# Kernel optimization log

Measured on AMD Instinct MI355X. Metric: run time of the kernel, lower is better.

Reference implementation:

```python
import jax, jax.numpy as jnp
import numpy as np

C = 343.0      # speed of sound (init kwarg c)
F = 16         # number of frequency channels (len(omega))
H = 128        # MLP hidden width
N = 131072     # collocation points


def _mlp(coords, W1, b1, W2, b2, W3, b3):
    # coords: [..., 3] -> [..., 2F] (first F = real part, last F = imag part)
    h = jnp.tanh(coords @ W1 + b1)
    h = jnp.tanh(h @ W2 + b2)
    return h @ W3 + b3


def setup_inputs() -> dict:
    key = jax.random.key(0)
    ks = jax.random.split(key, 4)
    inputs = jax.random.normal(ks[0], (N, 3), dtype=jnp.float32)
    # omega = 2*pi*f for f = 100..1600 Hz (matches init kwarg list)
    omega = 2.0 * jnp.pi * 100.0 * jnp.arange(1, F + 1, dtype=jnp.float32)
    s_in = 1.0 / np.sqrt(3.0)
    s_h = 1.0 / np.sqrt(float(H))
    W1 = jax.random.normal(ks[1], (3, H), dtype=jnp.float32) * s_in
    b1 = jnp.zeros((H,), dtype=jnp.float32)
    W2 = jax.random.normal(ks[2], (H, H), dtype=jnp.float32) * s_h
    b2 = jnp.zeros((H,), dtype=jnp.float32)
    W3 = jax.random.normal(ks[3], (H, 2 * F), dtype=jnp.float32) * s_h
    b3 = jnp.zeros((2 * F,), dtype=jnp.float32)
    return {"inputs": inputs, "omega": omega, "W1": W1, "b1": b1,
            "W2": W2, "b2": b2, "W3": W3, "b3": b3}


def reference(inputs, omega, W1, b1, W2, b2, W3, b3):
    # Pointwise network R^3 -> R^{2F} (real/imag stacked).
    f = lambda c3: _mlp(c3, W1, b1, W2, b2, W3, b3)

    # u: complex pressure per point per frequency, [N, F]
    out = _mlp(inputs, W1, b1, W2, b2, W3, b3)           # [N, 2F]
    u = out[:, :F] + 1j * out[:, F:]

    # Full spatial Hessian per point via forward-over-reverse AD (fused
    # replacement for the torch per-channel autograd.grad loop).
    hess = jax.vmap(jax.jacfwd(jax.jacrev(f)))(inputs)   # [N, 2F, 3, 3]
    lap_ri = jnp.einsum('nfii->nf', hess)                # diagonal trace = Laplacian
    lap = lap_ri[:, :F] + 1j * lap_ri[:, F:]             # [N, F] complex

    # PDE residual skips channel 0, exactly as the torch loop (i+1 indexing).
    k2 = (omega[1:] / C) ** 2                            # [F-1]
    residual = lap[:, 1:] + k2 * u[:, 1:]                # [N, F-1]

    # mean over channels then over batch == global mean of |residual|^2
    return jnp.mean(jnp.abs(residual) ** 2)
```

## Files before the change

### kernel.cpp

```cpp
#include <hip/hip_runtime.h>
#include <math.h>

#ifndef __has_builtin
#define __has_builtin(x) 0
#endif

#define NPTS   131072
#define FCH    16
#define CSND   343.0f
#define PB     32
#define BLOCK  256
#define GRID   512
#define NBLK   (NPTS / PB)

typedef _Float16 half8 __attribute__((ext_vector_type(8)));
typedef _Float16 half2v __attribute__((ext_vector_type(2)));
typedef float    f32x4 __attribute__((ext_vector_type(4)));

static __device__ __forceinline__ unsigned pack2(float a, float b) {
#if __has_builtin(__builtin_amdgcn_cvt_pkrtz)
  return __builtin_bit_cast(unsigned, __builtin_amdgcn_cvt_pkrtz(a, b));
#else
  half2v v; v[0] = (_Float16)a; v[1] = (_Float16)b;
  return __builtin_bit_cast(unsigned, v);
#endif
}

static __device__ __forceinline__ float mytanh(float x) {
#if __has_builtin(__builtin_amdgcn_exp2f)
  float e = __builtin_amdgcn_exp2f(2.885390082f * x);
#else
  float e = __expf(2.0f * x);
#endif
  return fmaf(-2.0f, __builtin_amdgcn_rcpf(e + 1.0f), 1.0f);
}


__global__ __launch_bounds__(BLOCK, 2) void helmholtz_kernel(
    const float* __restrict__ x,
    const float* __restrict__ omega,
    const float* __restrict__ W1,
    const float* __restrict__ b1,
    const float* __restrict__ W2,
    const float* __restrict__ b2,
    const float* __restrict__ W3,
    const float* __restrict__ b3,
    float* __restrict__ out)
{
  __shared__ unsigned s_A[160 * 64];
  __shared__ unsigned s_HG[32 * 128];

  const int tid  = threadIdx.x;
  const int w    = tid >> 6;
  const int l    = tid & 63;
  const int col  = l & 15;
  const int quad = l >> 4;
  const int ph   = w >> 1;
  const int nh   = w & 1;

  const int pA = tid >> 4;
  const int g  = tid & 15;
  float wx[8], wy[8], wz[8], bB[8];
#pragma unroll
  for (int u = 0; u < 8; u++) {
    int unit = 8 * g + u;
    wx[u] = W1[unit]; wy[u] = W1[128 + unit]; wz[u] = W1[256 + unit];
    bB[u] = b1[unit];
  }

  half8 w2f[4][4];
#pragma unroll
  for (int t4 = 0; t4 < 4; t4++) {
    const int n = 64 * nh + 16 * t4 + col;
#pragma unroll
    for (int ks = 0; ks < 4; ks++) {
      half8 f;
#pragma unroll
      for (int j8 = 0; j8 < 8; j8++)
        f[j8] = (_Float16)W2[(ks * 32 + (quad << 3) + j8) * 128 + n];
      w2f[t4][ks] = f;
    }
  }
  half8 w3f[4];
#pragma unroll
  for (int ks = 0; ks < 4; ks++) {
    half8 f;
#pragma unroll
    for (int j8 = 0; j8 < 8; j8++) {
      int kap = ks * 32 + (quad << 3) + j8;
      int q   = kap >> 1;
      int j   = 64 * (q >> 5) + 32 * ((q >> 4) & 1) + 16 * (kap & 1) + (q & 15);
      f[j8] = (_Float16)W3[j * 32 + 16 * nh + col];
    }
    w3f[ks] = f;
  }

  float b2r[4];
#pragma unroll
  for (int t4 = 0; t4 < 4; t4++) b2r[t4] = b2[64 * nh + 16 * t4 + col];
  float k2v = 0.0f;
  if (col >= 1) {
    float om = omega[col] * (1.0f / CSND);
    k2v = om * om;
  }
  const float b3v = b3[16 * nh + col];

  float wsum = 0.0f;
  float xr[2][3];

  auto loadX = [&](int blk) {
    const float* xb = x + (size_t)blk * PB * 3;
#pragma unroll
    for (int hp = 0; hp < 2; hp++) {
      int p = pA + 16 * hp;
      xr[hp][0] = xb[3 * p]; xr[hp][1] = xb[3 * p + 1]; xr[hp][2] = xb[3 * p + 2];
    }
  };

  auto phaseA = [&]() {
    const int cbase = (g ^ pA) << 2;
    float wq[8];
#pragma unroll
    for (int u = 0; u < 8; u++)
      wq[u] = fmaf(wx[u], wx[u], fmaf(wy[u], wy[u], wz[u] * wz[u]));
#pragma unroll
    for (int hp = 0; hp < 2; hp++) {
      int p = pA + 16 * hp;
      float x0 = xr[hp][0], x1 = xr[hp][1], x2 = xr[hp][2];
      float t[8], s[8];
#pragma unroll
      for (int u = 0; u < 8; u++) {
        float z = fmaf(x0, wx[u], fmaf(x1, wy[u], fmaf(x2, wz[u], bB[u])));
        t[u] = mytanh(z);
        s[u] = 1.0f - t[u] * t[u];
      }
      uint4 q;
      q = make_uint4(pack2(t[0], t[1]), pack2(t[2], t[3]),
                     pack2(t[4], t[5]), pack2(t[6], t[7]));
      *(uint4*)&s_A[(p)       * 64 + cbase] = q;
      q = make_uint4(pack2(s[0]*wx[0], s[1]*wx[1]), pack2(s[2]*wx[2], s[3]*wx[3]),
                     pack2(s[4]*wx[4], s[5]*wx[5]), pack2(s[6]*wx[6], s[7]*wx[7]));
      *(uint4*)&s_A[(32 + p)  * 64 + cbase] = q;
      q = make_uint4(pack2(s[0]*wy[0], s[1]*wy[1]), pack2(s[2]*wy[2], s[3]*wy[3]),
                     pack2(s[4]*wy[4], s[5]*wy[5]), pack2(s[6]*wy[6], s[7]*wy[7]));
      *(uint4*)&s_A[(64 + p)  * 64 + cbase] = q;
      q = make_uint4(pack2(s[0]*wz[0], s[1]*wz[1]), pack2(s[2]*wz[2], s[3]*wz[3]),
                     pack2(s[4]*wz[4], s[5]*wz[5]), pack2(s[6]*wz[6], s[7]*wz[7]));
      *(uint4*)&s_A[(96 + p)  * 64 + cbase] = q;
      float c[8];
#pragma unroll
      for (int u = 0; u < 8; u++) c[u] = -2.0f * t[u] * s[u] * wq[u];
      q = make_uint4(pack2(c[0], c[1]), pack2(c[2], c[3]),
                     pack2(c[4], c[5]), pack2(c[6], c[7]));
      *(uint4*)&s_A[(128 + p) * 64 + cbase] = q;
    }
  };

  auto phaseDE = [&]() {
    const int pbase = (16 * ph + col) * 128;
    f32x4 dy = (f32x4){0.0f, 0.0f, 0.0f, 0.0f};
    f32x4 dl = (f32x4){0.0f, 0.0f, 0.0f, 0.0f};
#pragma unroll
    for (int ks = 0; ks < 4; ks++) {
      int pos = ((((ks << 2) + quad) ^ col) << 2);
      half8 afy = *(const half8*)&s_HG[pbase + pos];
      half8 afl = *(const half8*)&s_HG[pbase + 64 + pos];
      dy = __builtin_amdgcn_mfma_f32_16x16x32_f16(afy, w3f[ks], dy, 0, 0, 0);
      dl = __builtin_amdgcn_mfma_f32_16x16x32_f16(afl, w3f[ks], dl, 0, 0, 0);
    }
    if (col >= 1) {
#pragma unroll
      for (int r = 0; r < 4; r++) {
        float yv  = dy[r] + b3v;
        float res = fmaf(k2v, yv, dl[r]);
        wsum += res * res;
      }
    }
  };

  loadX(blockIdx.x);
  bool first = true;
  for (int blk = blockIdx.x; blk < NBLK; blk += gridDim.x) {
    if (!first) phaseDE();
    first = false;
    phaseA();
    __syncthreads();

    int nblk = blk + (int)gridDim.x;
    if (nblk < NBLK) loadX(nblk);

    f32x4 bsum[4], acch[4], accc[4];
    {
      f32x4 accd[3][4];
#pragma unroll
      for (int d = 0; d < 3; d++)
#pragma unroll
        for (int t4 = 0; t4 < 4; t4++)
          accd[d][t4] = (f32x4){0.0f, 0.0f, 0.0f, 0.0f};
#pragma unroll
      for (int d = 0; d < 3; d++) {
        const int rb = ((d + 1) * 32 + 16 * ph + col) * 64;
#pragma unroll
        for (int ks = 0; ks < 4; ks++) {
          half8 af = *(const half8*)&s_A[rb + ((((ks << 2) + quad) ^ col) << 2)];
          accd[d][0] = __builtin_amdgcn_mfma_f32_16x16x32_f16(af, w2f[0][ks], accd[d][0], 0, 0, 0);
          accd[d][1] = __builtin_amdgcn_mfma_f32_16x16x32_f16(af, w2f[1][ks], accd[d][1], 0, 0, 0);
          accd[d][2] = __builtin_amdgcn_mfma_f32_16x16x32_f16(af, w2f[2][ks], accd[d][2], 0, 0, 0);
          accd[d][3] = __builtin_amdgcn_mfma_f32_16x16x32_f16(af, w2f[3][ks], accd[d][3], 0, 0, 0);
        }
      }
#pragma unroll
      for (int t4 = 0; t4 < 4; t4++)
        bsum[t4] = accd[0][t4] * accd[0][t4] + accd[1][t4] * accd[1][t4]
                 + accd[2][t4] * accd[2][t4];
    }
    {
#pragma unroll
      for (int t4 = 0; t4 < 4; t4++) {
        acch[t4] = (f32x4){0.0f, 0.0f, 0.0f, 0.0f};
        accc[t4] = (f32x4){0.0f, 0.0f, 0.0f, 0.0f};
      }
      const int rb0 = (16 * ph + col) * 64;
      const int rb4 = (128 + 16 * ph + col) * 64;
#pragma unroll
      for (int ks = 0; ks < 4; ks++) {
        int pos = ((((ks << 2) + quad) ^ col) << 2);
        half8 afh = *(const half8*)&s_A[rb0 + pos];
        half8 afc = *(const half8*)&s_A[rb4 + pos];
        acch[0] = __builtin_amdgcn_mfma_f32_16x16x32_f16(afh, w2f[0][ks], acch[0], 0, 0, 0);
        acch[1] = __builtin_amdgcn_mfma_f32_16x16x32_f16(afh, w2f[1][ks], acch[1], 0, 0, 0);
        acch[2] = __builtin_amdgcn_mfma_f32_16x16x32_f16(afh, w2f[2][ks], acch[2], 0, 0, 0);
        acch[3] = __builtin_amdgcn_mfma_f32_16x16x32_f16(afh, w2f[3][ks], acch[3], 0, 0, 0);
        accc[0] = __builtin_amdgcn_mfma_f32_16x16x32_f16(afc, w2f[0][ks], accc[0], 0, 0, 0);
        accc[1] = __builtin_amdgcn_mfma_f32_16x16x32_f16(afc, w2f[1][ks], accc[1], 0, 0, 0);
        accc[2] = __builtin_amdgcn_mfma_f32_16x16x32_f16(afc, w2f[2][ks], accc[2], 0, 0, 0);
        accc[3] = __builtin_amdgcn_mfma_f32_16x16x32_f16(afc, w2f[3][ks], accc[3], 0, 0, 0);
      }
    }

#pragma unroll
    for (int r = 0; r < 4; r++) {
      int p = 16 * ph + (quad << 2) + r;
      float t2[4], gg[4];
#pragma unroll
      for (int t4 = 0; t4 < 4; t4++) {
        float z2 = acch[t4][r] + b2r[t4];
        float t  = mytanh(z2);
        float s2 = 1.0f - t * t;
        t2[t4] = t;
        gg[t4] = s2 * (accc[t4][r] - 2.0f * t * bsum[t4][r]);
      }
      int pb = p * 128;
#pragma unroll
      for (int pr = 0; pr < 2; pr++) {
        int q   = 32 * nh + 16 * pr + col;
        int pos = (((q >> 2) ^ (p & 15)) << 2) + (q & 3);
        s_HG[pb + pos]      = pack2(t2[2 * pr], t2[2 * pr + 1]);
        s_HG[pb + 64 + pos] = pack2(gg[2 * pr], gg[2 * pr + 1]);
      }
    }
    __syncthreads();
  }
  phaseDE();

#pragma unroll
  for (int off = 32; off > 0; off >>= 1)
    wsum += __shfl_down(wsum, off, 64);
  if (l == 0)
    atomicAdd(out, wsum * (1.0f / ((float)NPTS * (float)(FCH - 1))));
}

extern "C" void kernel_launch(void* const* d_in, const int* in_sizes, int n_in,
                              void* d_out, int out_size, void* d_ws, size_t ws_size,
                              hipStream_t stream) {
  const float* x     = (const float*)d_in[0];
  const float* omega = (const float*)d_in[1];
  const float* W1    = (const float*)d_in[2];
  const float* b1    = (const float*)d_in[3];
  const float* W2    = (const float*)d_in[4];
  const float* b2    = (const float*)d_in[5];
  const float* W3    = (const float*)d_in[6];
  const float* b3    = (const float*)d_in[7];
  float* out = (float*)d_out;

  (void)hipMemsetAsync(out, 0, sizeof(float), stream);
  helmholtz_kernel<<<GRID, BLOCK, 0, stream>>>(x, omega, W1, b1, W2, b2, W3, b3, out);
}
```

Before: 122.1 us.

## Use packed fp16 math in layer-1 derivatives, stagger block starts, shrink accumulators

Layer-1 derivative terms (1-t^2, s*w, -2*t*s*|w|^2) are now computed with packed half2 arithmetic on pre-packed weights instead of per-element fp32 math followed by packing. This cuts VALU instruction count in phase A. The second-layer Jacobian accumulation is restructured to sum squares per direction, so only one set of four accumulators is live instead of three sets, reducing register pressure. Alternating groups of 256 blocks also sleep briefly at kernel start to stagger their phases, and the fp16 derivative math slightly reduces precision.

After: 119.9 us. About the same (-1.8%).

```diff
diff --git a/kernel.cpp b/kernel.cpp
--- a/kernel.cpp
+++ b/kernel.cpp
@@ -17,14 +17,18 @@
 typedef _Float16 half2v __attribute__((ext_vector_type(2)));
 typedef float    f32x4 __attribute__((ext_vector_type(4)));
 
-static __device__ __forceinline__ unsigned pack2(float a, float b) {
+static __device__ __forceinline__ half2v pk2h(float a, float b) {
 #if __has_builtin(__builtin_amdgcn_cvt_pkrtz)
-  return __builtin_bit_cast(unsigned, __builtin_amdgcn_cvt_pkrtz(a, b));
+  return __builtin_bit_cast(half2v, __builtin_amdgcn_cvt_pkrtz(a, b));
 #else
   half2v v; v[0] = (_Float16)a; v[1] = (_Float16)b;
-  return __builtin_bit_cast(unsigned, v);
+  return v;
 #endif
 }
+static __device__ __forceinline__ unsigned pack2(float a, float b) {
+  return __builtin_bit_cast(unsigned, pk2h(a, b));
+}
+#define U32(h) __builtin_bit_cast(unsigned, (h))
 
 static __device__ __forceinline__ float mytanh(float x) {
 #if __has_builtin(__builtin_amdgcn_exp2f)
@@ -50,6 +54,11 @@
   __shared__ unsigned s_A[160 * 64];
   __shared__ unsigned s_HG[32 * 128];
 
+  if ((blockIdx.x >> 8) & 1) {
+#pragma unroll
+    for (int i = 0; i < 3; i++) __builtin_amdgcn_s_sleep(56);
+  }
+
   const int tid  = threadIdx.x;
   const int w    = tid >> 6;
   const int l    = tid & 63;
@@ -67,6 +76,17 @@
     wx[u] = W1[unit]; wy[u] = W1[128 + unit]; wz[u] = W1[256 + unit];
     bB[u] = b1[unit];
   }
+  half2v wxp[4], wyp[4], wzp[4], wqm[4];
+#pragma unroll
+  for (int j = 0; j < 4; j++) {
+    wxp[j] = pk2h(wx[2*j], wx[2*j+1]);
+    wyp[j] = pk2h(wy[2*j], wy[2*j+1]);
+    wzp[j] = pk2h(wz[2*j], wz[2*j+1]);
+    float wq0 = fmaf(wx[2*j],   wx[2*j],   fmaf(wy[2*j],   wy[2*j],   wz[2*j]   * wz[2*j]));
+    float wq1 = fmaf(wx[2*j+1], wx[2*j+1], fmaf(wy[2*j+1], wy[2*j+1], wz[2*j+1] * wz[2*j+1]));
+    wqm[j] = pk2h(-2.0f * wq0, -2.0f * wq1);
+  }
+  const half2v hone = {(_Float16)1.0f, (_Float16)1.0f};
 
   half8 w2f[4][4];
 #pragma unroll
@@ -119,39 +139,38 @@
 
   auto phaseA = [&]() {
     const int cbase = (g ^ pA) << 2;
-    float wq[8];
-#pragma unroll
-    for (int u = 0; u < 8; u++)
-      wq[u] = fmaf(wx[u], wx[u], fmaf(wy[u], wy[u], wz[u] * wz[u]));
 #pragma unroll
     for (int hp = 0; hp < 2; hp++) {
       int p = pA + 16 * hp;
       float x0 = xr[hp][0], x1 = xr[hp][1], x2 = xr[hp][2];
-      float t[8], s[8];
+      float t[8];
 #pragma unroll
       for (int u = 0; u < 8; u++) {
         float z = fmaf(x0, wx[u], fmaf(x1, wy[u], fmaf(x2, wz[u], bB[u])));
         t[u] = mytanh(z);
-        s[u] = 1.0f - t[u] * t[u];
+      }
+      half2v tp[4], sp[4];
+#pragma unroll
+      for (int j = 0; j < 4; j++) {
+        tp[j] = pk2h(t[2*j], t[2*j+1]);
+        sp[j] = hone - tp[j] * tp[j];
       }
       uint4 q;
-      q = make_uint4(pack2(t[0], t[1]), pack2(t[2], t[3]),
-                     pack2(t[4], t[5]), pack2(t[6], t[7]));
+      q = make_uint4(U32(tp[0]), U32(tp[1]), U32(tp[2]), U32(tp[3]));
       *(uint4*)&s_A[(p)       * 64 + cbase] = q;
-      q = make_uint4(pack2(s[0]*wx[0], s[1]*wx[1]), pack2(s[2]*wx[2], s[3]*wx[3]),
-                     pack2(s[4]*wx[4], s[5]*wx[5]), pack2(s[6]*wx[6], s[7]*wx[7]));
+      q = make_uint4(U32(sp[0]*wxp[0]), U32(sp[1]*wxp[1]),
+                     U32(sp[2]*wxp[2]), U32(sp[3]*wxp[3]));
       *(uint4*)&s_A[(32 + p)  * 64 + cbase] = q;
-      q = make_uint4(pack2(s[0]*wy[0], s[1]*wy[1]), pack2(s[2]*wy[2], s[3]*wy[3]),
-                     pack2(s[4]*wy[4], s[5]*wy[5]), pack2(s[6]*wy[6], s[7]*wy[7]));
+      q = make_uint4(U32(sp[0]*wyp[0]), U32(sp[1]*wyp[1]),
+                     U32(sp[2]*wyp[2]), U32(sp[3]*wyp[3]));
       *(uint4*)&s_A[(64 + p)  * 64 + cbase] = q;
-      q = make_uint4(pack2(s[0]*wz[0], s[1]*wz[1]), pack2(s[2]*wz[2], s[3]*wz[3]),
-                     pack2(s[4]*wz[4], s[5]*wz[5]), pack2(s[6]*wz[6], s[7]*wz[7]));
+      q = make_uint4(U32(sp[0]*wzp[0]), U32(sp[1]*wzp[1]),
+                     U32(sp[2]*wzp[2]), U32(sp[3]*wzp[3]));
       *(uint4*)&s_A[(96 + p)  * 64 + cbase] = q;
-      float c[8];
-#pragma unroll
-      for (int u = 0; u < 8; u++) c[u] = -2.0f * t[u] * s[u] * wq[u];
-      q = make_uint4(pack2(c[0], c[1]), pack2(c[2], c[3]),
-                     pack2(c[4], c[5]), pack2(c[6], c[7]));
+      half2v cp[4];
+#pragma unroll
+      for (int j = 0; j < 4; j++) cp[j] = (tp[j] * sp[j]) * wqm[j];
+      q = make_uint4(U32(cp[0]), U32(cp[1]), U32(cp[2]), U32(cp[3]));
       *(uint4*)&s_A[(128 + p) * 64 + cbase] = q;
     }
   };
@@ -190,36 +209,34 @@
     if (nblk < NBLK) loadX(nblk);
 
     f32x4 bsum[4], acch[4], accc[4];
+#pragma unroll
+    for (int t4 = 0; t4 < 4; t4++)
+      bsum[t4] = (f32x4){0.0f, 0.0f, 0.0f, 0.0f};
+#pragma unroll
+    for (int d = 0; d < 3; d++) {
+      f32x4 accd[4];
+#pragma unroll
+      for (int t4 = 0; t4 < 4; t4++)
+        accd[t4] = (f32x4){0.0f, 0.0f, 0.0f, 0.0f};
+      const int rb = ((d + 1) * 32 + 16 * ph + col) * 64;
+#pragma unroll
+      for (int ks = 0; ks < 4; ks++) {
+        half8 af = *(const half8*)&s_A[rb + ((((ks << 2) + quad) ^ col) << 2)];
+        accd[0] = __builtin_amdgcn_mfma_f32_16x16x32_f16(af, w2f[0][ks], accd[0], 0, 0, 0);
+        accd[1] = __builtin_amdgcn_mfma_f32_16x16x32_f16(af, w2f[1][ks], accd[1], 0, 0, 0);
+        accd[2] = __builtin_amdgcn_mfma_f32_16x16x32_f16(af, w2f[2][ks], accd[2], 0, 0, 0);
+        accd[3] = __builtin_amdgcn_mfma_f32_16x16x32_f16(af, w2f[3][ks], accd[3], 0, 0, 0);
+      }
+#pragma unroll
+      for (int t4 = 0; t4 < 4; t4++)
+        bsum[t4] += accd[t4] * accd[t4];
+    }
+#pragma unroll
+    for (int t4 = 0; t4 < 4; t4++) {
+      acch[t4] = (f32x4){0.0f, 0.0f, 0.0f, 0.0f};
+      accc[t4] = (f32x4){0.0f, 0.0f, 0.0f, 0.0f};
+    }
     {
-      f32x4 accd[3][4];
-#pragma unroll
-      for (int d = 0; d < 3; d++)
-#pragma unroll
-        for (int t4 = 0; t4 < 4; t4++)
-          accd[d][t4] = (f32x4){0.0f, 0.0f, 0.0f, 0.0f};
-#pragma unroll
-      for (int d = 0; d < 3; d++) {
-        const int rb = ((d + 1) * 32 + 16 * ph + col) * 64;
-#pragma unroll
-        for (int ks = 0; ks < 4; ks++) {
-          half8 af = *(const half8*)&s_A[rb + ((((ks << 2) + quad) ^ col) << 2)];
-          accd[d][0] = __builtin_amdgcn_mfma_f32_16x16x32_f16(af, w2f[0][ks], accd[d][0], 0, 0, 0);
-          accd[d][1] = __builtin_amdgcn_mfma_f32_16x16x32_f16(af, w2f[1][ks], accd[d][1], 0, 0, 0);
-          accd[d][2] = __builtin_amdgcn_mfma_f32_16x16x32_f16(af, w2f[2][ks], accd[d][2], 0, 0, 0);
-          accd[d][3] = __builtin_amdgcn_mfma_f32_16x16x32_f16(af, w2f[3][ks], accd[d][3], 0, 0, 0);
-        }
-      }
-#pragma unroll
-      for (int t4 = 0; t4 < 4; t4++)
-        bsum[t4] = accd[0][t4] * accd[0][t4] + accd[1][t4] * accd[1][t4]
-                 + accd[2][t4] * accd[2][t4];
-    }
-    {
-#pragma unroll
-      for (int t4 = 0; t4 < 4; t4++) {
-        acch[t4] = (f32x4){0.0f, 0.0f, 0.0f, 0.0f};
-        accc[t4] = (f32x4){0.0f, 0.0f, 0.0f, 0.0f};
-      }
       const int rb0 = (16 * ph + col) * 64;
       const int rb4 = (128 + 16 * ph + col) * 64;
 #pragma unroll
```
